# Optimization experiments

Hardware: AMD Instinct MI355X
Metric: run time of the kernel (lower is better)

The kernel has to match this reference:

```python
import jax, jax.numpy as jnp
import numpy as np

IN_FEATURES = 512
OUT_FEATURES = 1024
ALPHA = 1.0
BATCH = 8192


def setup_inputs() -> dict:
    key = jax.random.key(0)
    kx, kw = jax.random.split(key)
    x = jax.random.normal(kx, (BATCH, IN_FEATURES), dtype=jnp.float32)
    # xavier_uniform for weight of shape (out, in): limit = sqrt(6/(fan_in+fan_out))
    limit = float(np.sqrt(6.0 / (IN_FEATURES + OUT_FEATURES)))
    weight = jax.random.uniform(kw, (OUT_FEATURES, IN_FEATURES), dtype=jnp.float32,
                                minval=-limit, maxval=limit)
    return {"x": x, "weight": weight}


def reference(x, weight):
    # dist: [B, K]
    x_sq = jnp.sum(x * x, axis=1, keepdims=True)            # [B, 1]
    w_sq = jnp.sum(weight * weight, axis=1)                  # [K]
    dist = x_sq + w_sq[None, :] - 2.0 * jnp.einsum('bd,kd->bk', x, weight)
    dist = jnp.maximum(dist, 0.0)
    # Student-t kernel soft assignment
    q = (1.0 + dist / ALPHA) ** (-(ALPHA + 1.0) / 2.0)       # [B, K]
    q = q / jnp.sum(q, axis=1, keepdims=True)                # row-normalize
    return q
```

## Files before the change

kernel.cpp:

```cpp
#include <hip/hip_runtime.h>
#include <hip/hip_bf16.h>

#define BATCH 8192
#define DIM   512
#define NCL   1024
#define ROWS  32
#define BK    32
#define NCH   (DIM / BK)
#define WPAD  40
#define XPAD  520

typedef __bf16 bf16x8 __attribute__((ext_vector_type(8)));
typedef float  f32x4  __attribute__((ext_vector_type(4)));

typedef const __attribute__((address_space(1))) void* gas_ptr;
typedef __attribute__((address_space(3))) void* las_ptr;

__device__ __forceinline__ unsigned short f2bf(float f) {
  union { float f; unsigned u; } v; v.f = f;
  unsigned r = v.u + 0x7fffu + ((v.u >> 16) & 1u);
  return (unsigned short)(r >> 16);
}
__device__ __forceinline__ unsigned pk(float a, float b) {
  return (unsigned)f2bf(a) | ((unsigned)f2bf(b) << 16);
}

__global__ __launch_bounds__(256) void prep_w(const float* __restrict__ w,
                                              __hip_bfloat16* __restrict__ wck,
                                              float* __restrict__ wsq) {
  int k    = blockIdx.x * 4 + (threadIdx.x >> 6);
  int lane = threadIdx.x & 63;
  const float4* wrow = (const float4*)(w + (size_t)k * DIM);
  float4 a = wrow[lane * 2 + 0];
  float4 b = wrow[lane * 2 + 1];
  float s = a.x*a.x + a.y*a.y + a.z*a.z + a.w*a.w
          + b.x*b.x + b.y*b.y + b.z*b.z + b.w*b.w;
  #pragma unroll
  for (int m = 32; m >= 1; m >>= 1) s += __shfl_xor(s, m, 64);
  if (lane == 0) wsq[k] = s;
  int c = lane >> 2;
  int j = (lane & 3) * 8;
  uint4 p = { pk(a.x, a.y), pk(a.z, a.w), pk(b.x, b.y), pk(b.z, b.w) };
  *(uint4*)(wck + (size_t)(c * NCL + k) * WPAD + j) = p;
}

__global__ __launch_bounds__(512) void fused(const float* __restrict__ x,
                                             const __hip_bfloat16* __restrict__ wck,
                                             const float* __restrict__ wsq,
                                             float* __restrict__ out) {
  __shared__ __hip_bfloat16 xs[ROWS * XPAD];
  __shared__ __hip_bfloat16 wt[NCL * WPAD];
  __shared__ float wsq_s[NCL];
  __shared__ float xsq_s[ROWS];
  __shared__ float red[ROWS][9];
  __shared__ float rowtot[ROWS];

  const int tid = threadIdx.x;
  const int r0  = blockIdx.x * ROWS;

  {
    int row = tid >> 4;
    int seg = tid & 15;
    const float4* src = (const float4*)(x + (size_t)(r0 + row) * DIM + seg * 32);
    float ss = 0.f;
    #pragma unroll
    for (int i = 0; i < 8; ++i) {
      float4 v = src[i];
      ss += v.x*v.x + v.y*v.y + v.z*v.z + v.w*v.w;
      uint2 p = { pk(v.x, v.y), pk(v.z, v.w) };
      *(uint2*)(xs + row * XPAD + seg * 32 + i * 4) = p;
    }
    ss += __shfl_xor(ss, 1, 64);
    ss += __shfl_xor(ss, 2, 64);
    ss += __shfl_xor(ss, 4, 64);
    ss += __shfl_xor(ss, 8, 64);
    if (seg == 0) xsq_s[row] = ss;
    wsq_s[tid]       = wsq[tid];
    wsq_s[tid + 512] = wsq[tid + 512];
  }

  const int wave = tid >> 6;
  const int lane = tid & 63;
  const int m16  = lane & 15;
  const int quad = lane >> 4;
  const int col0 = wave * 128;

  f32x4 acc[2][8];
  #pragma unroll
  for (int rt = 0; rt < 2; ++rt)
    #pragma unroll
    for (int ct = 0; ct < 8; ++ct)
      acc[rt][ct] = (f32x4){0.f, 0.f, 0.f, 0.f};

  for (int c = 0; c < NCH; ++c) {
    {
      const char* g = (const char*)wck + (size_t)c * (NCL * WPAD * 2);
      #pragma unroll
      for (int it = 0; it < 10; ++it) {
        int off = (it * 512 + tid) * 16;
        __builtin_amdgcn_global_load_lds((gas_ptr)(g + off), (las_ptr)((char*)wt + off), 16, 0, 0);
      }
    }
    __syncthreads();

    bf16x8 a0 = *(const bf16x8*)(xs + ( 0 + m16) * XPAD + c * BK + quad * 8);
    bf16x8 a1 = *(const bf16x8*)(xs + (16 + m16) * XPAD + c * BK + quad * 8);
    #pragma unroll
    for (int ct = 0; ct < 8; ++ct) {
      bf16x8 bf = *(const bf16x8*)(wt + (col0 + ct * 16 + m16) * WPAD + quad * 8);
      acc[0][ct] = __builtin_amdgcn_mfma_f32_16x16x32_bf16(a0, bf, acc[0][ct], 0, 0, 0);
      acc[1][ct] = __builtin_amdgcn_mfma_f32_16x16x32_bf16(a1, bf, acc[1][ct], 0, 0, 0);
    }
    __syncthreads();
  }

  float part[2][4];
  #pragma unroll
  for (int rt = 0; rt < 2; ++rt)
    #pragma unroll
    for (int i = 0; i < 4; ++i) part[rt][i] = 0.f;

  #pragma unroll
  for (int rt = 0; rt < 2; ++rt) {
    float xq[4];
    #pragma unroll
    for (int i = 0; i < 4; ++i) xq[i] = xsq_s[rt * 16 + quad * 4 + i];
    #pragma unroll
    for (int ct = 0; ct < 8; ++ct) {
      float wq = wsq_s[col0 + ct * 16 + m16];
      #pragma unroll
      for (int i = 0; i < 4; ++i) {
        float dist = fmaxf(xq[i] + wq - 2.f * acc[rt][ct][i], 0.f);
        float qu = 1.f / (1.f + dist);
        acc[rt][ct][i] = qu;
        part[rt][i] += qu;
      }
    }
  }
  #pragma unroll
  for (int rt = 0; rt < 2; ++rt)
    #pragma unroll
    for (int i = 0; i < 4; ++i) {
      float s = part[rt][i];
      s += __shfl_xor(s, 1, 64);
      s += __shfl_xor(s, 2, 64);
      s += __shfl_xor(s, 4, 64);
      s += __shfl_xor(s, 8, 64);
      part[rt][i] = s;
    }
  if (m16 == 0) {
    #pragma unroll
    for (int rt = 0; rt < 2; ++rt)
      #pragma unroll
      for (int i = 0; i < 4; ++i)
        red[rt * 16 + quad * 4 + i][wave] = part[rt][i];
  }
  __syncthreads();
  if (tid < ROWS) {
    float t = 0.f;
    #pragma unroll
    for (int w2 = 0; w2 < 8; ++w2) t += red[tid][w2];
    rowtot[tid] = 1.f / t;
  }
  __syncthreads();
  #pragma unroll
  for (int rt = 0; rt < 2; ++rt) {
    #pragma unroll
    for (int i = 0; i < 4; ++i) {
      int r = rt * 16 + quad * 4 + i;
      float inv = rowtot[r];
      float* orow = out + (size_t)(r0 + r) * NCL + col0 + m16;
      #pragma unroll
      for (int ct = 0; ct < 8; ++ct)
        orow[ct * 16] = acc[rt][ct][i] * inv;
    }
  }
}

extern "C" void kernel_launch(void* const* d_in, const int* in_sizes, int n_in,
                              void* d_out, int out_size, void* d_ws, size_t ws_size,
                              hipStream_t stream) {
  const float* x = (const float*)d_in[0];
  const float* w = (const float*)d_in[1];
  __hip_bfloat16* wck = (__hip_bfloat16*)d_ws;
  float* wsq = (float*)((char*)d_ws + (size_t)NCH * NCL * WPAD * 2);
  float* out = (float*)d_out;

  hipLaunchKernelGGL(prep_w, dim3(NCL / 4), dim3(256), 0, stream, w, wck, wsq);
  hipLaunchKernelGGL(fused, dim3(BATCH / ROWS), dim3(512), 0, stream, x, wck, wsq, out);
}
```

Measured before the change: 104.5 us.

## Read weight fragments directly from global and store x in MFMA-fragment LDS layout

Weight chunks are no longer staged through LDS with global_load_lds; each wave loads its bf16 B fragments straight from global (L2-resident, unpadded layout), which removes the per-chunk barriers. The x tile is stored in LDS in an MFMA-fragment-ordered layout so A operands are contiguous per lane. LDS use drops sharply, which may raise occupancy, but each wave now issues its own global loads with no prefetch or overlap, so latency may be exposed.

After: 104.1 us. About the same (-0.3%).

```diff
diff --git a/kernel.cpp b/kernel.cpp
--- a/kernel.cpp
+++ b/kernel.cpp
@@ -7,14 +7,9 @@
 #define ROWS  32
 #define BK    32
 #define NCH   (DIM / BK)
-#define WPAD  40
-#define XPAD  520
 
 typedef __bf16 bf16x8 __attribute__((ext_vector_type(8)));
 typedef float  f32x4  __attribute__((ext_vector_type(4)));
-
-typedef const __attribute__((address_space(1))) void* gas_ptr;
-typedef __attribute__((address_space(3))) void* las_ptr;
 
 __device__ __forceinline__ unsigned short f2bf(float f) {
   union { float f; unsigned u; } v; v.f = f;
@@ -41,15 +36,14 @@
   int c = lane >> 2;
   int j = (lane & 3) * 8;
   uint4 p = { pk(a.x, a.y), pk(a.z, a.w), pk(b.x, b.y), pk(b.z, b.w) };
-  *(uint4*)(wck + (size_t)(c * NCL + k) * WPAD + j) = p;
+  *(uint4*)(wck + ((size_t)c * NCL + k) * BK + j) = p;
 }
 
 __global__ __launch_bounds__(512) void fused(const float* __restrict__ x,
                                              const __hip_bfloat16* __restrict__ wck,
                                              const float* __restrict__ wsq,
                                              float* __restrict__ out) {
-  __shared__ __hip_bfloat16 xs[ROWS * XPAD];
-  __shared__ __hip_bfloat16 wt[NCL * WPAD];
+  __shared__ __align__(16) __hip_bfloat16 xs2[NCH * 2 * 512];
   __shared__ float wsq_s[NCL];
   __shared__ float xsq_s[ROWS];
   __shared__ float red[ROWS][9];
@@ -61,14 +55,16 @@
   {
     int row = tid >> 4;
     int seg = tid & 15;
-    const float4* src = (const float4*)(x + (size_t)(r0 + row) * DIM + seg * 32);
+    int rt  = row >> 4, m = row & 15;
+    const float4* src = (const float4*)(x + (size_t)(r0 + row) * DIM + seg * BK);
+    __hip_bfloat16* dst = xs2 + (seg * 2 + rt) * 512 + m * 8;
     float ss = 0.f;
     #pragma unroll
     for (int i = 0; i < 8; ++i) {
       float4 v = src[i];
       ss += v.x*v.x + v.y*v.y + v.z*v.z + v.w*v.w;
       uint2 p = { pk(v.x, v.y), pk(v.z, v.w) };
-      *(uint2*)(xs + row * XPAD + seg * 32 + i * 4) = p;
+      *(uint2*)(dst + (i >> 1) * 128 + (i & 1) * 4) = p;
     }
     ss += __shfl_xor(ss, 1, 64);
     ss += __shfl_xor(ss, 2, 64);
@@ -92,26 +88,19 @@
     for (int ct = 0; ct < 8; ++ct)
       acc[rt][ct] = (f32x4){0.f, 0.f, 0.f, 0.f};
 
+  __syncthreads();
+
+  #pragma unroll 2
   for (int c = 0; c < NCH; ++c) {
-    {
-      const char* g = (const char*)wck + (size_t)c * (NCL * WPAD * 2);
-      #pragma unroll
-      for (int it = 0; it < 10; ++it) {
-        int off = (it * 512 + tid) * 16;
-        __builtin_amdgcn_global_load_lds((gas_ptr)(g + off), (las_ptr)((char*)wt + off), 16, 0, 0);
-      }
-    }
-    __syncthreads();
-
-    bf16x8 a0 = *(const bf16x8*)(xs + ( 0 + m16) * XPAD + c * BK + quad * 8);
-    bf16x8 a1 = *(const bf16x8*)(xs + (16 + m16) * XPAD + c * BK + quad * 8);
+    bf16x8 a0 = *(const bf16x8*)(xs2 + (c * 2 + 0) * 512 + lane * 8);
+    bf16x8 a1 = *(const bf16x8*)(xs2 + (c * 2 + 1) * 512 + lane * 8);
+    const __hip_bfloat16* wp = wck + ((size_t)c * NCL + col0 + m16) * BK + quad * 8;
     #pragma unroll
     for (int ct = 0; ct < 8; ++ct) {
-      bf16x8 bf = *(const bf16x8*)(wt + (col0 + ct * 16 + m16) * WPAD + quad * 8);
+      bf16x8 bf = *(const bf16x8*)(wp + ct * (16 * BK));
       acc[0][ct] = __builtin_amdgcn_mfma_f32_16x16x32_bf16(a0, bf, acc[0][ct], 0, 0, 0);
       acc[1][ct] = __builtin_amdgcn_mfma_f32_16x16x32_bf16(a1, bf, acc[1][ct], 0, 0, 0);
     }
-    __syncthreads();
   }
 
   float part[2][4];
@@ -183,7 +172,7 @@
   const float* x = (const float*)d_in[0];
   const float* w = (const float*)d_in[1];
   __hip_bfloat16* wck = (__hip_bfloat16*)d_ws;
-  float* wsq = (float*)((char*)d_ws + (size_t)NCH * NCL * WPAD * 2);
+  float* wsq = (float*)((char*)d_ws + (size_t)NCH * NCL * BK * 2);
   float* out = (float*)d_out;
 
   hipLaunchKernelGGL(prep_w, dim3(NCL / 4), dim3(256), 0, stream, w, wck, wsq);
```
